# Optimization experiments

Hardware: AMD Instinct MI355X
Metric: run time of the kernel (lower is better)

Reference implementation:

```python
import jax, jax.numpy as jnp
import numpy as np

SPS_AMPLIFY = 1.5
SPS_DAMPEN = 0.3
SPS_DEEP_QUESTION = 0.1
SPS_EXCLAIM = 0.85
SPS_QUESTION = 0.25
SPS_SUPER_EXCLAIM = 0.95

B, S, D = 4, 2048, 1024
NUM_HEADS = 16
HEAD_DIM = D // NUM_HEADS
SCALE = HEAD_DIM ** (-0.5)


def sps_pro(x):
    """Piecewise elementwise modulation based on sigmoid(x) bands."""
    xn = jax.nn.sigmoid(x)
    # bands: xn>0.95 -> 2.0 ; 0.85<xn<=0.95 -> 1.5 ; xn<0.1 -> 0.1 ;
    #        0.1<=xn<0.25 -> 0.3 ; else -> 1.0
    mult = jnp.where(
        xn > SPS_SUPER_EXCLAIM, 2.0,
        jnp.where(xn > SPS_EXCLAIM, SPS_AMPLIFY,
                  jnp.where(xn < SPS_DEEP_QUESTION, 0.1,
                            jnp.where(xn < SPS_QUESTION, SPS_DAMPEN, 1.0))))
    return x * mult


def setup_inputs() -> dict:
    key = jax.random.key(0)
    k0, k1, k2, k3, k4 = jax.random.split(key, 5)
    s = 1.0 / np.sqrt(D)
    return {
        "x": jax.random.normal(k0, (B, S, D), dtype=jnp.float32),
        "W_qkv": jax.random.uniform(k1, (D, 3 * D), dtype=jnp.float32, minval=-s, maxval=s),
        "b_qkv": jax.random.uniform(k2, (3 * D,), dtype=jnp.float32, minval=-s, maxval=s),
        "W_proj": jax.random.uniform(k3, (D, D), dtype=jnp.float32, minval=-s, maxval=s),
        "b_proj": jax.random.uniform(k4, (D,), dtype=jnp.float32, minval=-s, maxval=s),
    }


def reference(x, W_qkv, b_qkv, W_proj, b_proj):
    qkv = jnp.einsum('bsd,de->bse', x, W_qkv) + b_qkv  # [B,S,3D]
    q, k, v = jnp.split(qkv, 3, axis=-1)               # each [B,S,D]
    attn = jnp.einsum('bsd,btd->bst', q, k) * SCALE    # [B,S,S]
    attn = sps_pro(attn)
    attn = jax.nn.softmax(attn, axis=-1)
    out = jnp.einsum('bst,btd->bsd', attn, v)          # [B,S,D]
    out = jnp.einsum('bsd,de->bse', out, W_proj) + b_proj
    return out
```

## Files before the change

### kernel.cpp

```cpp
#include <hip/hip_runtime.h>
#include <hip/hip_bf16.h>
#include <hip/hip_fp16.h>
#include <stdint.h>

typedef __attribute__((ext_vector_type(8))) _Float16 f16x8;
typedef __attribute__((ext_vector_type(4))) float f32x4;

__device__ __forceinline__ void async16(void* lds, const void* g) {
  __builtin_amdgcn_global_load_lds(
      (const __attribute__((address_space(1))) void*)g,
      (__attribute__((address_space(3))) void*)lds, 16, 0, 0);
}

__device__ __forceinline__ uint16_t f2h_u(float f) {
  union { __half h; uint16_t u; } c;
  c.h = __float2half(f);
  return c.u;
}

__global__ __launch_bounds__(256)
void conv_f2h(const float* __restrict__ in, uint16_t* __restrict__ out, int n4) {
  int i = blockIdx.x * 256 + threadIdx.x;
  if (i >= n4) return;
  float4 v = ((const float4*)in)[i];
  ushort4 o;
  o.x = f2h_u(v.x); o.y = f2h_u(v.y); o.z = f2h_u(v.z); o.w = f2h_u(v.w);
  ((ushort4*)out)[i] = o;
}

__global__ __launch_bounds__(256)
void trans_f2h(const float* __restrict__ in, uint16_t* __restrict__ out,
               int ldin, int ldout) {
  __shared__ float t[64][65];
  const int tx = threadIdx.x & 63, ty = threadIdx.x >> 6;
  const int r0 = blockIdx.y * 64, c0 = blockIdx.x * 64;
#pragma unroll
  for (int i = 0; i < 16; ++i)
    t[ty + i * 4][tx] = in[(size_t)(r0 + ty + i * 4) * ldin + c0 + tx];
  __syncthreads();
#pragma unroll
  for (int i = 0; i < 16; ++i)
    out[(size_t)(c0 + ty + i * 4) * ldout + r0 + tx] = f2h_u(t[tx][ty + i * 4]);
}

template <int EPI>
__global__ __launch_bounds__(512, 2)
void gemm8p(const uint16_t* __restrict__ A, const uint16_t* __restrict__ B,
            void* __restrict__ Cv, void* __restrict__ Cv2,
            const float* __restrict__ bias,
            int nT, int lda, int ldb, int ldc,
            long long strA, long long strB, long long strC) {
  extern __shared__ uint16_t lds_u16[];

  const int gx = gridDim.x, gy = gridDim.y;
  const int nwg = gx * gy * gridDim.z;
  const int fid = blockIdx.x + gx * (blockIdx.y + gy * blockIdx.z);
  const int fs = (fid & 7) * (nwg >> 3) + (fid >> 3);
  const int bx = fs % gx;
  const int by = (fs / gx) % gy;
  const int bz = fs / (gx * gy);

  const int tid = threadIdx.x;
  const int l = tid & 63;
  const int w = tid >> 6;
  const int wm = w >> 2, wn = w & 3;
  const int l15 = l & 15, l4 = l >> 4;
  const int rowBase = bx * 256, colBase = by * 256;
  const uint16_t* Ag = A + (size_t)bz * strA;
  const uint16_t* Bg = B + (size_t)bz * strB;

  const uint16_t* sA[2][2];
  const uint16_t* sB[2][2];
#pragma unroll
  for (int u = 0; u < 2; ++u) {
    int c = tid + (u << 9);
    int cs = c ^ ((c >> 3) & 7);
    int row = cs >> 3, kc = (cs & 7) * 8;
    sA[0][u] = Ag + (size_t)(rowBase + row) * lda + kc;
    sA[1][u] = Ag + (size_t)(rowBase + 128 + row) * lda + kc;
    sB[0][u] = Bg + (size_t)(colBase + row) * ldb + kc;
    sB[1][u] = Bg + (size_t)(colBase + 128 + row) * ldb + kc;
  }

  f32x4 acc[8][4];
#pragma unroll
  for (int m = 0; m < 8; ++m)
#pragma unroll
    for (int n = 0; n < 4; ++n)
      acc[m][n] = (f32x4){0.f, 0.f, 0.f, 0.f};

#define SH_A(buf, h, koff)                                                     \
  {                                                                            \
    const uint32_t d_ = (buf)*32768u + (h)*8192u;                              \
    async16(&lds_u16[d_ + (size_t)tid * 8], sA[h][0] + (koff));                \
    async16(&lds_u16[d_ + (size_t)(tid + 512) * 8], sA[h][1] + (koff));        \
  }
#define SH_B(buf, h, koff)                                                     \
  {                                                                            \
    const uint32_t d_ = (buf)*32768u + 16384u + (h)*8192u;                     \
    async16(&lds_u16[d_ + (size_t)tid * 8], sB[h][0] + (koff));                \
    async16(&lds_u16[d_ + (size_t)(tid + 512) * 8], sB[h][1] + (koff));        \
  }
#define RD_A(dst, buf, mh)                                                     \
  _Pragma("unroll") for (int mr = 0; mr < 4; ++mr) {                           \
    const int lr = (mh)*64 + mr * 16 + l15;                                    \
    const char* hb = (const char*)lds_u16 + (buf)*65536 + wm * 16384;          \
    _Pragma("unroll") for (int ks = 0; ks < 2; ++ks)                           \
      dst[mr][ks] = *(const f16x8*)(hb + lr * 128 +                            \
                    ((ks * 64 + l4 * 16) ^ ((lr & 7) << 4)));                  \
  }
#define RD_B(dst, buf, nh)                                                     \
  _Pragma("unroll") for (int nr = 0; nr < 2; ++nr) {                           \
    const int lr = (wn & 1) * 64 + (nh)*32 + nr * 16 + l15;                    \
    const char* hb = (const char*)lds_u16 + (buf)*65536 + 32768 +              \
                     (wn >> 1) * 16384;                                        \
    _Pragma("unroll") for (int ks = 0; ks < 2; ++ks)                           \
      dst[nr][ks] = *(const f16x8*)(hb + lr * 128 +                            \
                    ((ks * 64 + l4 * 16) ^ ((lr & 7) << 4)));                  \
  }
#define MM(m0, n0, AF, BF)                                                     \
  __builtin_amdgcn_s_setprio(1);                                               \
  _Pragma("unroll") for (int ks = 0; ks < 2; ++ks)                             \
  _Pragma("unroll") for (int mr = 0; mr < 4; ++mr)                             \
  _Pragma("unroll") for (int nr = 0; nr < 2; ++nr)                             \
    acc[(m0) + mr][(n0) + nr] = __builtin_amdgcn_mfma_f32_16x16x32_f16(        \
        AF[mr][ks], BF[nr][ks], acc[(m0) + mr][(n0) + nr], 0, 0, 0);           \
  __builtin_amdgcn_s_setprio(0);
#define VMC(n) asm volatile("s_waitcnt vmcnt(" #n ")" ::: "memory");
#define BAR() __builtin_amdgcn_s_barrier();

  SH_A(0, 0, 0) SH_A(0, 1, 0) SH_B(0, 0, 0) SH_B(0, 1, 0)
  SH_B(1, 0, 64) SH_B(1, 1, 64)
  VMC(4)
  BAR()

  const int nIter = nT >> 1;
  for (int i = 0; i < nIter; ++i) {
    const int e2 = 2 * i + 2, o = 2 * i + 1, o2 = 2 * i + 3;
    const int ke2 = e2 << 6, ko = o << 6, ko2 = o2 << 6;
    f16x8 a0[4][2], a1[4][2], b0[2][2], b1[2][2];
    RD_A(a0, 0, 0) RD_B(b0, 0, 0)
    SH_A(1, 0, ko)
    BAR()
    MM(0, 0, a0, b0)
    RD_B(b1, 0, 1)
    SH_A(1, 1, ko)
    BAR()
    MM(0, 2, a0, b1)
    RD_A(a1, 0, 1)
    if (e2 < nT) SH_B(0, 0, ke2)
    BAR()
    MM(4, 2, a1, b1)
    if (e2 < nT) { SH_B(0, 1, ke2) VMC(4) } else { VMC(0) }
    BAR()
    MM(4, 0, a1, b0)
    RD_A(a0, 1, 0) RD_B(b0, 1, 0)
    if (e2 < nT) SH_A(0, 0, ke2)
    BAR()
    MM(0, 0, a0, b0)
    RD_B(b1, 1, 1)
    if (e2 < nT) SH_A(0, 1, ke2)
    BAR()
    MM(0, 2, a0, b1)
    RD_A(a1, 1, 1)
    if (o2 < nT) SH_B(1, 0, ko2)
    BAR()
    MM(4, 2, a1, b1)
    if (o2 < nT) { SH_B(1, 1, ko2) }
    if (i + 1 < nIter) { if (o2 < nT) { VMC(4) } else { VMC(0) } }
    BAR()
    MM(4, 0, a1, b0)
  }
#undef SH_A
#undef SH_B
#undef RD_A
#undef RD_B
#undef MM
#undef VMC
#undef BAR

  if (EPI == 0) {
    uint16_t* qd = (uint16_t*)Cv;
    uint16_t* kd = (uint16_t*)Cv2;
#pragma unroll
    for (int ni = 0; ni < 4; ++ni) {
      const int gcol = colBase + wn * 64 + ni * 16 + l15;
      const float bv = bias[gcol];
      uint16_t* base = (gcol < 1024 ? qd : kd) + (gcol & 1023);
#pragma unroll
      for (int mi = 0; mi < 8; ++mi)
#pragma unroll
        for (int j = 0; j < 4; ++j) {
          const int grow = rowBase + wm * 128 + mi * 16 + l4 * 4 + j;
          base[(size_t)(grow >> 11) * 2097152 + (size_t)(grow & 2047) * 1024] =
              f2h_u(acc[mi][ni][j] + bv);
        }
    }
  }
}

template <int EPI>
__global__ __launch_bounds__(256, 2)
void gemm_mb(const uint16_t* __restrict__ A, const uint16_t* __restrict__ B,
             void* __restrict__ Cv, const float* __restrict__ bias,
             float* __restrict__ rowsum,
             int nT, int lda, int ldb, int ldc,
             long long strA, long long strB, long long strC) {
  extern __shared__ uint16_t lds_u16[];

  const int gx = gridDim.x, gy = gridDim.y;
  const int nwg = gx * gy * gridDim.z;
  const int fid = blockIdx.x + gx * (blockIdx.y + gy * blockIdx.z);
  const int fs = (fid & 7) * (nwg >> 3) + (fid >> 3);
  const int bx = fs % gx;
  const int by = (fs / gx) % gy;
  const int bz = fs / (gx * gy);

  const int tid = threadIdx.x;
  const int l = tid & 63;
  const int w = tid >> 6;
  const int wm = w >> 1, wn = w & 1;
  const int l15 = l & 15, l4 = l >> 4;
  const int rowBase = bx * 128, colBase = by * 128;
  const uint16_t* Ag = A + (size_t)bz * strA;
  const uint16_t* Bg = B + (size_t)bz * strB;

  const uint16_t* pA[4];
  const uint16_t* pB[4];
#pragma unroll
  for (int u = 0; u < 4; ++u) {
    int c = tid + (u << 8);
    int cs = c ^ ((c >> 3) & 7);
    pA[u] = Ag + (size_t)(rowBase + (cs >> 3)) * lda + (cs & 7) * 8;
    pB[u] = Bg + (size_t)(colBase + (cs >> 3)) * ldb + (cs & 7) * 8;
  }

  f32x4 acc[4][4];
#pragma unroll
  for (int m = 0; m < 4; ++m)
#pragma unroll
    for (int n = 0; n < 4; ++n)
      acc[m][n] = (f32x4){0.f, 0.f, 0.f, 0.f};

#define STAGE(t2, s2)                                                          \
  {                                                                            \
    const int kb_ = (t2) << 6;                                                 \
    uint16_t* dA_ = lds_u16 + (s2)*16384;                                      \
    uint16_t* dB_ = dA_ + 8192;                                                \
    _Pragma("unroll") for (int u = 0; u < 4; ++u) {                            \
      async16(&dA_[(size_t)(tid + (u << 8)) * 8], pA[u] + kb_);                \
      async16(&dB_[(size_t)(tid + (u << 8)) * 8], pB[u] + kb_);                \
    }                                                                          \
  }

  STAGE(0, 0)
  asm volatile("s_waitcnt vmcnt(0)" ::: "memory");
  __builtin_amdgcn_s_barrier();

  for (int t = 0; t < nT; ++t) {
    const int s = t & 1;
    if (t + 1 < nT) STAGE(t + 1, s ^ 1)
    const uint16_t* As = lds_u16 + s * 16384;
    const uint16_t* Bs = As + 8192;
#pragma unroll
    for (int ks = 0; ks < 2; ++ks) {
      f16x8 af[4], bf[4];
#pragma unroll
      for (int m = 0; m < 4; ++m) {
        const int r = wm * 64 + m * 16 + l15;
        const int byt = r * 128 + ((ks * 64 + l4 * 16) ^ ((r & 7) << 4));
        af[m] = *(const f16x8*)((const char*)As + byt);
      }
#pragma unroll
      for (int n = 0; n < 4; ++n) {
        const int r = wn * 64 + n * 16 + l15;
        const int byt = r * 128 + ((ks * 64 + l4 * 16) ^ ((r & 7) << 4));
        bf[n] = *(const f16x8*)((const char*)Bs + byt);
      }
      __builtin_amdgcn_s_setprio(1);
#pragma unroll
      for (int m = 0; m < 4; ++m)
#pragma unroll
        for (int n = 0; n < 4; ++n)
          acc[m][n] = __builtin_amdgcn_mfma_f32_16x16x32_f16(af[m], bf[n], acc[m][n], 0, 0, 0);
      __builtin_amdgcn_s_setprio(0);
    }
    if (t + 1 < nT) {
      asm volatile("s_waitcnt vmcnt(0)" ::: "memory");
      __builtin_amdgcn_s_barrier();
    }
  }
#undef STAGE

  const int orow0 = rowBase + wm * 64 + l4 * 4;
  const int ocol0 = colBase + wn * 64 + l15;
  if (EPI == 2) {
    uint16_t* C = (uint16_t*)Cv + (size_t)bz * strC;
#pragma unroll
    for (int m = 0; m < 4; ++m)
#pragma unroll
      for (int j = 0; j < 4; ++j) {
        const int d = orow0 + m * 16 + j;
        const float bv = bias[d];
#pragma unroll
        for (int n = 0; n < 4; ++n)
          C[(size_t)d * ldc + ocol0 + n * 16] = f2h_u(acc[m][n][j] + bv);
      }
  } else if (EPI == 5) {
    uint16_t* C = (uint16_t*)Cv + (size_t)bz * strC;
    float* rs_b = rowsum + (size_t)bz * 2048;
#pragma unroll
    for (int m = 0; m < 4; ++m)
#pragma unroll
      for (int j = 0; j < 4; ++j) {
        const int grow = orow0 + m * 16 + j;
        float rs = 0.f;
#pragma unroll
        for (int n = 0; n < 4; ++n) {
          float xs = acc[m][n][j] * 0.125f;
          float mult = (xs > 2.94443897916644f) ? 2.0f
                     : (xs > 1.73460105538811f) ? 1.5f
                     : (xs < -2.19722457733622f) ? 0.1f
                     : (xs < -1.09861228866811f) ? 0.3f
                                                 : 1.0f;
          float e = __expf(fminf(xs * mult, 19.0f) - 8.0f);
          C[(size_t)grow * ldc + ocol0 + n * 16] = f2h_u(e);
          rs += e;
        }
        rs += __shfl_xor(rs, 1);
        rs += __shfl_xor(rs, 2);
        rs += __shfl_xor(rs, 4);
        rs += __shfl_xor(rs, 8);
        if (l15 == 0) atomicAdd(&rs_b[grow], rs);
      }
  } else if (EPI == 6) {
    uint16_t* C = (uint16_t*)Cv + (size_t)bz * strC;
    const float* rs_b = rowsum + (size_t)bz * 2048;
#pragma unroll
    for (int m = 0; m < 4; ++m)
#pragma unroll
      for (int j = 0; j < 4; ++j) {
        const int grow = orow0 + m * 16 + j;
        const float inv = 1.0f / rs_b[grow];
#pragma unroll
        for (int n = 0; n < 4; ++n)
          C[(size_t)grow * ldc + ocol0 + n * 16] = f2h_u(acc[m][n][j] * inv);
      }
  } else {
    float* C = (float*)Cv;
#pragma unroll
    for (int n = 0; n < 4; ++n) {
      const float bv = bias[ocol0 + n * 16];
#pragma unroll
      for (int m = 0; m < 4; ++m)
#pragma unroll
        for (int j = 0; j < 4; ++j)
          C[(size_t)(orow0 + m * 16 + j) * ldc + ocol0 + n * 16] = acc[m][n][j] + bv;
    }
  }
}

extern "C" void kernel_launch(void* const* d_in, const int* in_sizes, int n_in,
                              void* d_out, int out_size, void* d_ws, size_t ws_size,
                              hipStream_t stream) {
  const float* x     = (const float*)d_in[0];
  const float* Wqkv  = (const float*)d_in[1];
  const float* bqkv  = (const float*)d_in[2];
  const float* Wproj = (const float*)d_in[3];
  const float* bproj = (const float*)d_in[4];
  float* out = (float*)d_out;

  char* ws = (char*)d_ws;
  size_t off = 0;
  auto alloc = [&](size_t bytes) -> void* {
    void* p = ws + off;
    off += (bytes + 255) & ~(size_t)255;
    return p;
  };
  uint16_t* xh     = (uint16_t*)alloc(8192ULL * 1024 * 2);
  uint16_t* WqkvT  = (uint16_t*)alloc(3072ULL * 1024 * 2);
  uint16_t* WpT    = (uint16_t*)alloc(1024ULL * 1024 * 2);
  uint16_t* qh     = (uint16_t*)alloc(4ULL * 2048 * 1024 * 2);
  uint16_t* kh     = (uint16_t*)alloc(4ULL * 2048 * 1024 * 2);
  uint16_t* vT     = (uint16_t*)alloc(4ULL * 1024 * 2048 * 2);
  uint16_t* Pm     = (uint16_t*)alloc(4ULL * 2048 * 2048 * 2);
  float*    rowsum = (float*)alloc(4ULL * 2048 * 4);
  uint16_t* ao     = xh;

  hipMemsetAsync(rowsum, 0, 4ULL * 2048 * 4, stream);
  conv_f2h<<<8192, 256, 0, stream>>>(x, xh, 2097152);
  trans_f2h<<<dim3(48, 16), 256, 0, stream>>>(Wqkv, WqkvT, 3072, 1024);
  trans_f2h<<<dim3(16, 16), 256, 0, stream>>>(Wproj, WpT, 1024, 1024);
  gemm8p<0><<<dim3(32, 8, 1), 512, 131072, stream>>>(
      xh, WqkvT, qh, kh, bqkv, 16, 1024, 1024, 0, 0, 0, 0);
  gemm_mb<2><<<dim3(8, 16, 4), 256, 65536, stream>>>(
      WqkvT + 2048ULL * 1024, xh, vT, bqkv + 2048, nullptr,
      16, 1024, 1024, 2048, 0, 2097152LL, 2097152LL);
  gemm_mb<5><<<dim3(16, 16, 4), 256, 65536, stream>>>(
      qh, kh, Pm, nullptr, rowsum, 16, 1024, 1024, 2048,
      2097152LL, 2097152LL, 4194304LL);
  gemm_mb<6><<<dim3(16, 8, 4), 256, 65536, stream>>>(
      Pm, vT, ao, nullptr, rowsum, 32, 2048, 2048, 1024,
      4194304LL, 2097152LL, 2097152LL);
  gemm_mb<4><<<dim3(64, 8, 1), 256, 65536, stream>>>(
      ao, WpT, out, bproj, nullptr, 16, 1024, 1024, 1024, 0, 0, 0);
}
```

Before: 207.0 us.

## Merge prep kernels into one launch and run QK projection on gemm_mb

Replaces the three conversion/transpose kernels with one `prep_all` kernel that picks its job from the block index. This removes launch gaps between the small prep steps. It also drops the 256x256 eight-wave `gemm8p` kernel and runs the Q/K projection through the 128x128 `gemm_mb` kernel with a new epilogue. That epilogue writes Q and K into one contiguous buffer, relying on `kh` being allocated right after `qh`. The smaller tiles give more workgroups but less operand reuse per tile than the hand-pipelined big-tile kernel.

```diff
diff --git a/kernel.cpp b/kernel.cpp
--- a/kernel.cpp
+++ b/kernel.cpp
@@ -19,183 +19,42 @@
 }
 
 __global__ __launch_bounds__(256)
-void conv_f2h(const float* __restrict__ in, uint16_t* __restrict__ out, int n4) {
-  int i = blockIdx.x * 256 + threadIdx.x;
-  if (i >= n4) return;
-  float4 v = ((const float4*)in)[i];
-  ushort4 o;
-  o.x = f2h_u(v.x); o.y = f2h_u(v.y); o.z = f2h_u(v.z); o.w = f2h_u(v.w);
-  ((ushort4*)out)[i] = o;
-}
-
-__global__ __launch_bounds__(256)
-void trans_f2h(const float* __restrict__ in, uint16_t* __restrict__ out,
-               int ldin, int ldout) {
-  __shared__ float t[64][65];
-  const int tx = threadIdx.x & 63, ty = threadIdx.x >> 6;
-  const int r0 = blockIdx.y * 64, c0 = blockIdx.x * 64;
-#pragma unroll
-  for (int i = 0; i < 16; ++i)
-    t[ty + i * 4][tx] = in[(size_t)(r0 + ty + i * 4) * ldin + c0 + tx];
-  __syncthreads();
-#pragma unroll
-  for (int i = 0; i < 16; ++i)
-    out[(size_t)(c0 + ty + i * 4) * ldout + r0 + tx] = f2h_u(t[tx][ty + i * 4]);
-}
-
-template <int EPI>
-__global__ __launch_bounds__(512, 2)
-void gemm8p(const uint16_t* __restrict__ A, const uint16_t* __restrict__ B,
-            void* __restrict__ Cv, void* __restrict__ Cv2,
-            const float* __restrict__ bias,
-            int nT, int lda, int ldb, int ldc,
-            long long strA, long long strB, long long strC) {
-  extern __shared__ uint16_t lds_u16[];
-
-  const int gx = gridDim.x, gy = gridDim.y;
-  const int nwg = gx * gy * gridDim.z;
-  const int fid = blockIdx.x + gx * (blockIdx.y + gy * blockIdx.z);
-  const int fs = (fid & 7) * (nwg >> 3) + (fid >> 3);
-  const int bx = fs % gx;
-  const int by = (fs / gx) % gy;
-  const int bz = fs / (gx * gy);
-
-  const int tid = threadIdx.x;
-  const int l = tid & 63;
-  const int w = tid >> 6;
-  const int wm = w >> 2, wn = w & 3;
-  const int l15 = l & 15, l4 = l >> 4;
-  const int rowBase = bx * 256, colBase = by * 256;
-  const uint16_t* Ag = A + (size_t)bz * strA;
-  const uint16_t* Bg = B + (size_t)bz * strB;
-
-  const uint16_t* sA[2][2];
-  const uint16_t* sB[2][2];
-#pragma unroll
-  for (int u = 0; u < 2; ++u) {
-    int c = tid + (u << 9);
-    int cs = c ^ ((c >> 3) & 7);
-    int row = cs >> 3, kc = (cs & 7) * 8;
-    sA[0][u] = Ag + (size_t)(rowBase + row) * lda + kc;
-    sA[1][u] = Ag + (size_t)(rowBase + 128 + row) * lda + kc;
-    sB[0][u] = Bg + (size_t)(colBase + row) * ldb + kc;
-    sB[1][u] = Bg + (size_t)(colBase + 128 + row) * ldb + kc;
-  }
-
-  f32x4 acc[8][4];
-#pragma unroll
-  for (int m = 0; m < 8; ++m)
-#pragma unroll
-    for (int n = 0; n < 4; ++n)
-      acc[m][n] = (f32x4){0.f, 0.f, 0.f, 0.f};
-
-#define SH_A(buf, h, koff)                                                     \
-  {                                                                            \
-    const uint32_t d_ = (buf)*32768u + (h)*8192u;                              \
-    async16(&lds_u16[d_ + (size_t)tid * 8], sA[h][0] + (koff));                \
-    async16(&lds_u16[d_ + (size_t)(tid + 512) * 8], sA[h][1] + (koff));        \
-  }
-#define SH_B(buf, h, koff)                                                     \
-  {                                                                            \
-    const uint32_t d_ = (buf)*32768u + 16384u + (h)*8192u;                     \
-    async16(&lds_u16[d_ + (size_t)tid * 8], sB[h][0] + (koff));                \
-    async16(&lds_u16[d_ + (size_t)(tid + 512) * 8], sB[h][1] + (koff));        \
-  }
-#define RD_A(dst, buf, mh)                                                     \
-  _Pragma("unroll") for (int mr = 0; mr < 4; ++mr) {                           \
-    const int lr = (mh)*64 + mr * 16 + l15;                                    \
-    const char* hb = (const char*)lds_u16 + (buf)*65536 + wm * 16384;          \
-    _Pragma("unroll") for (int ks = 0; ks < 2; ++ks)                           \
-      dst[mr][ks] = *(const f16x8*)(hb + lr * 128 +                            \
-                    ((ks * 64 + l4 * 16) ^ ((lr & 7) << 4)));                  \
-  }
-#define RD_B(dst, buf, nh)                                                     \
-  _Pragma("unroll") for (int nr = 0; nr < 2; ++nr) {                           \
-    const int lr = (wn & 1) * 64 + (nh)*32 + nr * 16 + l15;                    \
-    const char* hb = (const char*)lds_u16 + (buf)*65536 + 32768 +              \
-                     (wn >> 1) * 16384;                                        \
-    _Pragma("unroll") for (int ks = 0; ks < 2; ++ks)                           \
-      dst[nr][ks] = *(const f16x8*)(hb + lr * 128 +                            \
-                    ((ks * 64 + l4 * 16) ^ ((lr & 7) << 4)));                  \
-  }
-#define MM(m0, n0, AF, BF)                                                     \
-  __builtin_amdgcn_s_setprio(1);                                               \
-  _Pragma("unroll") for (int ks = 0; ks < 2; ++ks)                             \
-  _Pragma("unroll") for (int mr = 0; mr < 4; ++mr)                             \
-  _Pragma("unroll") for (int nr = 0; nr < 2; ++nr)                             \
-    acc[(m0) + mr][(n0) + nr] = __builtin_amdgcn_mfma_f32_16x16x32_f16(        \
-        AF[mr][ks], BF[nr][ks], acc[(m0) + mr][(n0) + nr], 0, 0, 0);           \
-  __builtin_amdgcn_s_setprio(0);
-#define VMC(n) asm volatile("s_waitcnt vmcnt(" #n ")" ::: "memory");
-#define BAR() __builtin_amdgcn_s_barrier();
-
-  SH_A(0, 0, 0) SH_A(0, 1, 0) SH_B(0, 0, 0) SH_B(0, 1, 0)
-  SH_B(1, 0, 64) SH_B(1, 1, 64)
-  VMC(4)
-  BAR()
-
-  const int nIter = nT >> 1;
-  for (int i = 0; i < nIter; ++i) {
-    const int e2 = 2 * i + 2, o = 2 * i + 1, o2 = 2 * i + 3;
-    const int ke2 = e2 << 6, ko = o << 6, ko2 = o2 << 6;
-    f16x8 a0[4][2], a1[4][2], b0[2][2], b1[2][2];
-    RD_A(a0, 0, 0) RD_B(b0, 0, 0)
-    SH_A(1, 0, ko)
-    BAR()
-    MM(0, 0, a0, b0)
-    RD_B(b1, 0, 1)
-    SH_A(1, 1, ko)
-    BAR()
-    MM(0, 2, a0, b1)
-    RD_A(a1, 0, 1)
-    if (e2 < nT) SH_B(0, 0, ke2)
-    BAR()
-    MM(4, 2, a1, b1)
-    if (e2 < nT) { SH_B(0, 1, ke2) VMC(4) } else { VMC(0) }
-    BAR()
-    MM(4, 0, a1, b0)
-    RD_A(a0, 1, 0) RD_B(b0, 1, 0)
-    if (e2 < nT) SH_A(0, 0, ke2)
-    BAR()
-    MM(0, 0, a0, b0)
-    RD_B(b1, 1, 1)
-    if (e2 < nT) SH_A(0, 1, ke2)
-    BAR()
-    MM(0, 2, a0, b1)
-    RD_A(a1, 1, 1)
-    if (o2 < nT) SH_B(1, 0, ko2)
-    BAR()
-    MM(4, 2, a1, b1)
-    if (o2 < nT) { SH_B(1, 1, ko2) }
-    if (i + 1 < nIter) { if (o2 < nT) { VMC(4) } else { VMC(0) } }
-    BAR()
-    MM(4, 0, a1, b0)
-  }
-#undef SH_A
-#undef SH_B
-#undef RD_A
-#undef RD_B
-#undef MM
-#undef VMC
-#undef BAR
-
-  if (EPI == 0) {
-    uint16_t* qd = (uint16_t*)Cv;
-    uint16_t* kd = (uint16_t*)Cv2;
-#pragma unroll
-    for (int ni = 0; ni < 4; ++ni) {
-      const int gcol = colBase + wn * 64 + ni * 16 + l15;
-      const float bv = bias[gcol];
-      uint16_t* base = (gcol < 1024 ? qd : kd) + (gcol & 1023);
-#pragma unroll
-      for (int mi = 0; mi < 8; ++mi)
-#pragma unroll
-        for (int j = 0; j < 4; ++j) {
-          const int grow = rowBase + wm * 128 + mi * 16 + l4 * 4 + j;
-          base[(size_t)(grow >> 11) * 2097152 + (size_t)(grow & 2047) * 1024] =
-              f2h_u(acc[mi][ni][j] + bv);
-        }
-    }
+void prep_all(const float* __restrict__ x, uint16_t* __restrict__ xh,
+              const float* __restrict__ Wqkv, uint16_t* __restrict__ WqkvT,
+              const float* __restrict__ Wproj, uint16_t* __restrict__ WpT) {
+  const int bid = blockIdx.x;
+  if (bid < 2048) {
+    const int base = bid * 256 + threadIdx.x;
+#pragma unroll
+    for (int k = 0; k < 4; ++k) {
+      const int i = base + k * 524288;
+      float4 v = ((const float4*)x)[i];
+      ushort4 o;
+      o.x = f2h_u(v.x); o.y = f2h_u(v.y); o.z = f2h_u(v.z); o.w = f2h_u(v.w);
+      ((ushort4*)xh)[i] = o;
+    }
+  } else {
+    __shared__ float t[64][65];
+    const float* in;
+    uint16_t* out;
+    int ldin, ldout, r0, c0;
+    if (bid < 2816) {
+      const int id = bid - 2048;
+      in = Wqkv; out = WqkvT; ldin = 3072; ldout = 1024;
+      c0 = (id % 48) * 64; r0 = (id / 48) * 64;
+    } else {
+      const int id = bid - 2816;
+      in = Wproj; out = WpT; ldin = 1024; ldout = 1024;
+      c0 = (id % 16) * 64; r0 = (id / 16) * 64;
+    }
+    const int tx = threadIdx.x & 63, ty = threadIdx.x >> 6;
+#pragma unroll
+    for (int i = 0; i < 16; ++i)
+      t[ty + i * 4][tx] = in[(size_t)(r0 + ty + i * 4) * ldin + c0 + tx];
+    __syncthreads();
+#pragma unroll
+    for (int i = 0; i < 16; ++i)
+      out[(size_t)(c0 + ty + i * 4) * ldout + r0 + tx] = f2h_u(t[tx][ty + i * 4]);
   }
 }
 
@@ -294,7 +153,23 @@
 
   const int orow0 = rowBase + wm * 64 + l4 * 4;
   const int ocol0 = colBase + wn * 64 + l15;
-  if (EPI == 2) {
+  if (EPI == 0) {
+    uint16_t* qd = (uint16_t*)Cv;
+#pragma unroll
+    for (int n = 0; n < 4; ++n) {
+      const int gcol = ocol0 + n * 16;
+      const float bv = bias[gcol];
+      uint16_t* base = qd + (gcol < 1024 ? 0 : 8388608) + (gcol & 1023);
+#pragma unroll
+      for (int m = 0; m < 4; ++m)
+#pragma unroll
+        for (int j = 0; j < 4; ++j) {
+          const int grow = orow0 + m * 16 + j;
+          base[(size_t)(grow >> 11) * 2097152 + (size_t)(grow & 2047) * 1024] =
+              f2h_u(acc[m][n][j] + bv);
+        }
+    }
+  } else if (EPI == 2) {
     uint16_t* C = (uint16_t*)Cv + (size_t)bz * strC;
 #pragma unroll
     for (int m = 0; m < 4; ++m)
@@ -386,18 +261,17 @@
   uint16_t* Pm     = (uint16_t*)alloc(4ULL * 2048 * 2048 * 2);
   float*    rowsum = (float*)alloc(4ULL * 2048 * 4);
   uint16_t* ao     = xh;
+  (void)kh;
 
   hipMemsetAsync(rowsum, 0, 4ULL * 2048 * 4, stream);
-  conv_f2h<<<8192, 256, 0, stream>>>(x, xh, 2097152);
-  trans_f2h<<<dim3(48, 16), 256, 0, stream>>>(Wqkv, WqkvT, 3072, 1024);
-  trans_f2h<<<dim3(16, 16), 256, 0, stream>>>(Wproj, WpT, 1024, 1024);
-  gemm8p<0><<<dim3(32, 8, 1), 512, 131072, stream>>>(
-      xh, WqkvT, qh, kh, bqkv, 16, 1024, 1024, 0, 0, 0, 0);
+  prep_all<<<3072, 256, 0, stream>>>(x, xh, Wqkv, WqkvT, Wproj, WpT);
+  gemm_mb<0><<<dim3(64, 16, 1), 256, 65536, stream>>>(
+      xh, WqkvT, qh, bqkv, nullptr, 16, 1024, 1024, 0, 0, 0, 0);
   gemm_mb<2><<<dim3(8, 16, 4), 256, 65536, stream>>>(
       WqkvT + 2048ULL * 1024, xh, vT, bqkv + 2048, nullptr,
       16, 1024, 1024, 2048, 0, 2097152LL, 2097152LL);
   gemm_mb<5><<<dim3(16, 16, 4), 256, 65536, stream>>>(
-      qh, kh, Pm, nullptr, rowsum, 16, 1024, 1024, 2048,
+      qh, qh + 8388608, Pm, nullptr, rowsum, 16, 1024, 1024, 2048,
       2097152LL, 2097152LL, 4194304LL);
   gemm_mb<6><<<dim3(16, 8, 4), 256, 65536, stream>>>(
       Pm, vT, ao, nullptr, rowsum, 32, 2048, 2048, 1024,
```

Result: no change. 210.4 us (+1.6%).
